# Kernel tuning notes

Hardware: AMD Instinct MI355X
Metric: run time of the kernel (lower is better)

The kernel has to match this reference:

```python
import jax, jax.numpy as jnp
import numpy as np

N_NODES = 100000


def gcn_conv(x, src, dst, ew, W, b):
    """PyG GCNConv: linear transform, add self-loops, symmetric degree
    normalization with edge weights, scatter-add aggregation, then bias."""
    n = x.shape[0]
    h = x @ W  # [N, out] transform BEFORE propagation (PyG order)
    # add self-loops with weight 1
    loop = jnp.arange(n, dtype=src.dtype)
    s = jnp.concatenate([src, loop])
    d = jnp.concatenate([dst, loop])
    w = jnp.concatenate([ew, jnp.ones((n,), dtype=ew.dtype)])
    # symmetric normalization: deg computed over incoming edge weights
    deg = jax.ops.segment_sum(w, d, num_segments=n)
    dinv = jnp.where(deg > 0, jax.lax.rsqrt(deg), 0.0)
    norm = dinv[s] * w * dinv[d]  # [E+N]
    msg = h[s] * norm[:, None]  # gather + scale
    out = jax.ops.segment_sum(msg, d, num_segments=n)  # scatter-add
    return out + b


def setup_inputs() -> dict:
    key = jax.random.key(0)
    k = jax.random.split(key, 6)
    N, E, F, H, C = N_NODES, 3200000, 512, 16, 40
    x = jax.random.normal(k[0], (N, F), dtype=jnp.float32)
    edge_index = jax.random.randint(k[1], (2, E), 0, N, dtype=jnp.int64)
    edge_weight = jax.random.uniform(k[2], (E,), dtype=jnp.float32)
    W1 = jax.random.normal(k[3], (F, H), dtype=jnp.float32) * (1.0 / np.sqrt(F))
    b1 = jnp.zeros((H,), dtype=jnp.float32)
    W2 = jax.random.normal(k[4], (H, C), dtype=jnp.float32) * (1.0 / np.sqrt(H))
    b2 = jnp.zeros((C,), dtype=jnp.float32)
    return {"x": x, "edge_index": edge_index, "edge_weight": edge_weight,
            "W1": W1, "b1": b1, "W2": W2, "b2": b2}


def reference(x, edge_index, edge_weight, W1, b1, W2, b2):
    src, dst = edge_index[0], edge_index[1]
    h = jax.nn.relu(gcn_conv(x, src, dst, edge_weight, W1, b1))
    # F.dropout with training=False (eval) is identity -> omitted
    h = gcn_conv(h, src, dst, edge_weight, W2, b2)
    return jax.nn.log_softmax(h, axis=1)
```

## Files before the change

### kernel.cpp

```cpp
#include <hip/hip_runtime.h>


#define NF 512
#define NH 16
#define NRANGE 32
#define NS2 32
#define RS 3125
#define EB 1024
#define GROWS 256
#define GK 16

__device__ __forceinline__ unsigned short f2bf(float f) {
    unsigned u = __float_as_uint(f);
    return (unsigned short)((u + 0x7fff + ((u >> 16) & 1)) >> 16);
}
__device__ __forceinline__ float bf2f(unsigned b) {
    return __uint_as_float(b << 16);
}


__global__ __launch_bounds__(256) void k_bincount(const int* __restrict__ dst,
                                                  int* __restrict__ bktcnt,
                                                  int E, int nblk) {
    __shared__ int cnt[NRANGE];
    if (threadIdx.x < NRANGE) cnt[threadIdx.x] = 0;
    __syncthreads();
    int b0 = blockIdx.x * EB;
#pragma unroll
    for (int j = 0; j < 4; ++j) {
        int e = b0 + j * 256 + threadIdx.x;
        if (e < E) atomicAdd(&cnt[dst[e] / RS], 1);
    }
    __syncthreads();
    if (threadIdx.x < NRANGE)
        bktcnt[threadIdx.x * nblk + blockIdx.x] = cnt[threadIdx.x];
}

__global__ __launch_bounds__(256) void k_scan_block(const int* __restrict__ in,
                                                    int* __restrict__ outp,
                                                    int* __restrict__ bsum, int n) {
    __shared__ int sh[256];
    int t = threadIdx.x, g = blockIdx.x * 256 + t;
    int v = (g < n) ? in[g] : 0;
    sh[t] = v; __syncthreads();
    for (int off = 1; off < 256; off <<= 1) {
        int a = (t >= off) ? sh[t - off] : 0;
        __syncthreads();
        sh[t] += a;
        __syncthreads();
    }
    if (g < n) outp[g] = sh[t] - v;
    if (t == 255) bsum[blockIdx.x] = sh[255];
}

__global__ __launch_bounds__(256) void k_sumscan(const int* __restrict__ partials,
                                                 const float* __restrict__ wpartials,
                                                 int* __restrict__ rowptr,
                                                 int* __restrict__ bsum,
                                                 float* __restrict__ dinv, int n) {
    __shared__ int sh[256];
    int t = threadIdx.x, g = blockIdx.x * 256 + t;
    int v = 0;
    if (g < n) {
        int r = g / RS, b = g - r * RS;
        size_t o = (size_t)(r * NS2) * RS + b;
        const int* p = partials + o;
        const float* wp = wpartials + o;
        float w = 1.0f;
#pragma unroll
        for (int s = 0; s < NS2; ++s) { v += p[s * RS]; w += wp[s * RS]; }
        dinv[g] = rsqrtf(w);
    }
    sh[t] = v; __syncthreads();
    for (int off = 1; off < 256; off <<= 1) {
        int a = (t >= off) ? sh[t - off] : 0;
        __syncthreads();
        sh[t] += a;
        __syncthreads();
    }
    if (g < n) rowptr[g] = sh[t] - v;
    if (t == 255) bsum[blockIdx.x] = sh[255];
}

__global__ __launch_bounds__(512) void k_scan_tops(int* __restrict__ bsum,
                                                   int* __restrict__ outp,
                                                   int nb, int n) {
    __shared__ int sh[512];
    int t = threadIdx.x;
    int v = (t < nb) ? bsum[t] : 0;
    sh[t] = v; __syncthreads();
    for (int off = 1; off < 512; off <<= 1) {
        int a = (t >= off) ? sh[t - off] : 0;
        __syncthreads();
        sh[t] += a;
        __syncthreads();
    }
    if (t < nb) bsum[t] = sh[t] - v;
    if (t == 511) outp[n] = sh[511];
}

__global__ __launch_bounds__(256) void k_scan_add(int* __restrict__ outp,
                                                  const int* __restrict__ bsum, int n) {
    int i = blockIdx.x * 256 + threadIdx.x;
    if (i < n) outp[i] += bsum[i >> 8];
}

__global__ __launch_bounds__(256) void k_binfill(const int* __restrict__ src,
                                                 const int* __restrict__ dst,
                                                 const float* __restrict__ ew,
                                                 const int* __restrict__ bktcnt,
                                                 const int* __restrict__ bsum2,
                                                 int2* __restrict__ bin,
                                                 int E, int nblk) {
    __shared__ int base[NRANGE];
    if (threadIdx.x < NRANGE) {
        int idx = threadIdx.x * nblk + blockIdx.x;
        base[threadIdx.x] = bktcnt[idx] + bsum2[idx >> 8];
    }
    __syncthreads();
    int b0 = blockIdx.x * EB;
#pragma unroll
    for (int j = 0; j < 4; ++j) {
        int e = b0 + j * 256 + threadIdx.x;
        if (e < E) {
            int d = dst[e];
            int r = d / RS;
            int pos = atomicAdd(&base[r], 1);
            bin[pos] = make_int2((src[e] << 12) | (d - r * RS),
                                 __float_as_int(ew[e]));
        }
    }
}

__device__ __forceinline__ int bkt_start(const int* bktcnt, const int* bsum2,
                                         int r, int nblk, int E) {
    if (r >= NRANGE) return E;
    int idx = r * nblk;
    return bktcnt[idx] + bsum2[idx >> 8];
}

__global__ __launch_bounds__(256) void k_hist2(const int2* __restrict__ bin,
                                               const int* __restrict__ bktcnt,
                                               const int* __restrict__ bsum2,
                                               int* __restrict__ partials,
                                               float* __restrict__ wpartials,
                                               int E, int nblk) {
    __shared__ int hist[RS];
    __shared__ float whist[RS];
    int r = blockIdx.x >> 5, s = blockIdx.x & (NS2 - 1);
    for (int t = threadIdx.x; t < RS; t += 256) { hist[t] = 0; whist[t] = 0.f; }
    __syncthreads();
    int b0 = bkt_start(bktcnt, bsum2, r, nblk, E);
    int b1 = bkt_start(bktcnt, bsum2, r + 1, nblk, E);
    int len = b1 - b0, ss = (len + NS2 - 1) / NS2;
    int cs = b0 + s * ss, ce = min(cs + ss, b1);
    for (int j = cs + threadIdx.x; j < ce; j += 256) {
        int2 p2 = bin[j];
        int dl = p2.x & 4095;
        atomicAdd(&hist[dl], 1);
        atomicAdd(&whist[dl], __int_as_float(p2.y));
    }
    __syncthreads();
    size_t o = (size_t)(r * NS2 + s) * RS;
    int* pp = partials + o;
    float* wpp = wpartials + o;
    for (int t = threadIdx.x; t < RS; t += 256) { pp[t] = hist[t]; wpp[t] = whist[t]; }
}

__global__ __launch_bounds__(256) void k_slicecur(int* __restrict__ partials,
                                                  const int* __restrict__ rowptr, int n) {
    int d = blockIdx.x * 256 + threadIdx.x;
    if (d >= n) return;
    int r = d / RS, b = d - r * RS;
    int* p = partials + (size_t)(r * NS2) * RS + b;
    int run = rowptr[d];
#pragma unroll
    for (int s = 0; s < NS2; ++s) {
        int c = p[s * RS];
        p[s * RS] = run;
        run += c;
    }
}

__global__ __launch_bounds__(256) void k_fill3(const int2* __restrict__ bin,
                                               const int* __restrict__ bktcnt,
                                               const int* __restrict__ bsum2,
                                               const int* __restrict__ partials,
                                               const float* __restrict__ dinv,
                                               unsigned* __restrict__ csr,
                                               int E, int nblk) {
    __shared__ int cur[RS];
    __shared__ float dv[RS];
    int r = blockIdx.x >> 5, s = blockIdx.x & (NS2 - 1);
    const int* cp = partials + (size_t)(r * NS2 + s) * RS;
    for (int t = threadIdx.x; t < RS; t += 256) {
        cur[t] = cp[t];
        dv[t] = dinv[r * RS + t];
    }
    __syncthreads();
    int b0 = bkt_start(bktcnt, bsum2, r, nblk, E);
    int b1 = bkt_start(bktcnt, bsum2, r + 1, nblk, E);
    int len = b1 - b0, ss = (len + NS2 - 1) / NS2;
    int cs = b0 + s * ss, ce = min(cs + ss, b1);
    for (int j = cs + threadIdx.x; j < ce; j += 256) {
        int2 p2 = bin[j];
        int dl = p2.x & 4095;
        int sn = p2.x >> 12;
        float nrm = dinv[sn] * __int_as_float(p2.y) * dv[dl];
        unsigned w15 = (unsigned)(nrm * 32767.0f + 0.5f);
        int pos = atomicAdd(&cur[dl], 1);
        csr[pos] = ((unsigned)sn << 15) | w15;
    }
}

__global__ __launch_bounds__(256) void k_gemm1(const float* __restrict__ x,
                                               const float* __restrict__ w1,
                                               unsigned short* __restrict__ h, int n) {
    __shared__ float wt[NF * NH];
    __shared__ float xs[2][GROWS * GK];
    for (int t = threadIdx.x; t < NF * NH; t += 256) {
        int k = t >> 4, f = t & 15;
        wt[(k >> 2) * 64 + (f << 2) + (k & 3)] = w1[t];
    }
    int rq = threadIdx.x >> 2;
    int fq = threadIdx.x & 3;
    int base = blockIdx.x * GROWS;
    float4 stage[4];
#define LOAD_CHUNK(kc)                                                        \
    _Pragma("unroll")                                                         \
    for (int li = 0; li < 4; ++li) {                                          \
        int idx = li * 256 + threadIdx.x;                                     \
        int row = idx >> 2, c4 = idx & 3;                                     \
        int rg = base + row; if (rg > n - 1) rg = n - 1;                      \
        stage[li] = *(const float4*)(x + (size_t)rg * NF + (kc) * GK + c4 * 4);\
    }
#define WRITE_CHUNK(b)                                                        \
    _Pragma("unroll")                                                         \
    for (int li = 0; li < 4; ++li) {                                          \
        int idx = li * 256 + threadIdx.x;                                     \
        int row = idx >> 2, c4 = idx & 3;                                     \
        int slot = (c4 + (row >> 2)) & 3;                                     \
        float* p = &xs[b][row * GK + slot * 4];                               \
        p[0] = stage[li].x; p[1] = stage[li].y;                               \
        p[2] = stage[li].z; p[3] = stage[li].w;                               \
    }
    float acc[4][4] = {{0.f}};
    LOAD_CHUNK(0)
    WRITE_CHUNK(0)
    __syncthreads();
    for (int kc = 0; kc < NF / GK; ++kc) {
        if (kc + 1 < NF / GK) { LOAD_CHUNK(kc + 1) }
        int b = kc & 1;
#pragma unroll
        for (int k4c = 0; k4c < GK / 4; ++k4c) {
            int k4 = kc * (GK / 4) + k4c;
            float4 wf[4];
#pragma unroll
            for (int c = 0; c < 4; ++c)
                wf[c] = *(const float4*)&wt[k4 * 64 + (fq * 4 + c) * 4];
#pragma unroll
            for (int i = 0; i < 4; ++i) {
                int row = rq * 4 + i;
                int slot = (k4c + rq) & 3;
                float4 xv = *(const float4*)&xs[b][row * GK + slot * 4];
#pragma unroll
                for (int c = 0; c < 4; ++c) {
                    acc[i][c] = fmaf(xv.x, wf[c].x, acc[i][c]);
                    acc[i][c] = fmaf(xv.y, wf[c].y, acc[i][c]);
                    acc[i][c] = fmaf(xv.z, wf[c].z, acc[i][c]);
                    acc[i][c] = fmaf(xv.w, wf[c].w, acc[i][c]);
                }
            }
        }
        if (kc + 1 < NF / GK) {
            __syncthreads();
            WRITE_CHUNK((kc + 1) & 1)
            __syncthreads();
        }
    }
#pragma unroll
    for (int i = 0; i < 4; ++i) {
        int r = base + rq * 4 + i;
        if (r < n) {
            ushort4 o;
            o.x = f2bf(acc[i][0]); o.y = f2bf(acc[i][1]);
            o.z = f2bf(acc[i][2]); o.w = f2bf(acc[i][3]);
            *(ushort4*)(h + (size_t)r * NH + fq * 4) = o;
        }
    }
#undef LOAD_CHUNK
#undef WRITE_CHUNK
}

template <bool RELU>
__global__ __launch_bounds__(256) void k_gatherT(const unsigned short* __restrict__ in,
                                                 const float* __restrict__ dinv,
                                                 const int* __restrict__ rowptr,
                                                 const unsigned* __restrict__ csr,
                                                 const float* __restrict__ b1,
                                                 unsigned short* __restrict__ out, int n) {
    int tid = blockIdx.x * 256 + threadIdx.x;
    int d = tid >> 3, l = tid & 7;
    if (d >= n) return;
    float di = dinv[d];
    unsigned self = *(const unsigned*)(in + (size_t)d * NH + 2 * l);
    float a0 = bf2f(self & 0xffffu) * di * di;
    float a1 = bf2f(self >> 16) * di * di;
    int e0 = rowptr[d], e1 = rowptr[d + 1];
    for (int j = e0; j < e1; ++j) {
        unsigned e = csr[j];
        float nrm = (float)(e & 32767u) * (1.0f / 32767.0f);
        unsigned pr = *(const unsigned*)(in + (size_t)(e >> 15) * NH + 2 * l);
        a0 = fmaf(bf2f(pr & 0xffffu), nrm, a0);
        a1 = fmaf(bf2f(pr >> 16), nrm, a1);
    }
    if (RELU) {
        a0 = fmaxf(a0 + b1[2 * l], 0.0f);
        a1 = fmaxf(a1 + b1[2 * l + 1], 0.0f);
    }
    unsigned pk = (unsigned)f2bf(a0) | ((unsigned)f2bf(a1) << 16);
    *(unsigned*)(out + (size_t)d * NH + 2 * l) = pk;
}

__global__ __launch_bounds__(256) void k_out(const unsigned short* __restrict__ agg,
                                             const float* __restrict__ w2,
                                             const float* __restrict__ b2,
                                             float* __restrict__ out, int n) {
    __shared__ float w2s[NH * 40];
    __shared__ float b2s[40];
    for (int t = threadIdx.x; t < NH * 40; t += 256) w2s[t] = w2[t];
    if (threadIdx.x < 40) b2s[threadIdx.x] = b2[threadIdx.x];
    __syncthreads();
    int i = blockIdx.x * 256 + threadIdx.x;
    if (i >= n) return;
    float v[NH];
    const uint4* ap = (const uint4*)(agg + (size_t)i * NH);
#pragma unroll
    for (int m = 0; m < 2; ++m) {
        uint4 q = ap[m];
        v[8 * m + 0] = bf2f(q.x & 0xffffu); v[8 * m + 1] = bf2f(q.x >> 16);
        v[8 * m + 2] = bf2f(q.y & 0xffffu); v[8 * m + 3] = bf2f(q.y >> 16);
        v[8 * m + 4] = bf2f(q.z & 0xffffu); v[8 * m + 5] = bf2f(q.z >> 16);
        v[8 * m + 6] = bf2f(q.w & 0xffffu); v[8 * m + 7] = bf2f(q.w >> 16);
    }
    float z[40];
#pragma unroll
    for (int c = 0; c < 40; ++c) {
        float a = b2s[c];
#pragma unroll
        for (int ff = 0; ff < NH; ++ff) a = fmaf(v[ff], w2s[ff * 40 + c], a);
        z[c] = a;
    }
    float mx = z[0];
#pragma unroll
    for (int c = 1; c < 40; ++c) mx = fmaxf(mx, z[c]);
    float sum = 0.0f;
#pragma unroll
    for (int c = 0; c < 40; ++c) sum += expf(z[c] - mx);
    float ls = mx + logf(sum);
    float4* op = (float4*)(out + (size_t)i * 40);
#pragma unroll
    for (int m = 0; m < 10; ++m) {
        float4 o;
        o.x = z[4 * m] - ls; o.y = z[4 * m + 1] - ls;
        o.z = z[4 * m + 2] - ls; o.w = z[4 * m + 3] - ls;
        op[m] = o;
    }
}

extern "C" void kernel_launch(void* const* d_in, const int* in_sizes, int n_in,
                              void* d_out, int out_size, void* d_ws, size_t ws_size,
                              hipStream_t stream) {
    const float* x  = (const float*)d_in[0];
    const int*   ei = (const int*)d_in[1];
    const float* ew = (const float*)d_in[2];
    const float* w1 = (const float*)d_in[3];
    const float* b1 = (const float*)d_in[4];
    const float* w2 = (const float*)d_in[5];
    const float* b2 = (const float*)d_in[6];
    float* out = (float*)d_out;

    int n = in_sizes[0] / NF;
    int E = in_sizes[2];
    const int* src = ei;
    const int* dst = ei + E;

    float*          ws        = (float*)d_ws;
    float*          dinv      = ws;
    int*            bsum      = (int*)(ws + 200000);
    int*            rowptr    = (int*)(ws + 201024);
    int*            bsum2     = (int*)(ws + 301056);
    int*            bktcnt    = (int*)(ws + 302080);
    int*            partials  = (int*)(ws + 402112);
    float*          wpartials = ws + 3602112;
    unsigned*       csr       = (unsigned*)(ws + 6802112);
    int2*           bin       = (int2*)(ws + 10002112);
    unsigned short* h         = (unsigned short*)(ws + 10002112);
    unsigned short* o1        = (unsigned short*)(ws + 10802112);

    int nblk  = (E + EB - 1) / EB;
    int ncnt  = NRANGE * nblk;
    int nb_c  = (ncnt + 255) / 256;
    int nb_n  = (n + 255) / 256;
    int nb_g8 = (n * 8 + 255) / 256;
    int nb_g  = (n + GROWS - 1) / GROWS;

    k_bincount<<<nblk, 256, 0, stream>>>(dst, bktcnt, E, nblk);
    k_scan_block<<<nb_c, 256, 0, stream>>>(bktcnt, bktcnt, bsum2, ncnt);
    k_scan_tops<<<1, 512, 0, stream>>>(bsum2, bktcnt, nb_c, ncnt);
    k_binfill<<<nblk, 256, 0, stream>>>(src, dst, ew, bktcnt, bsum2, bin, E, nblk);
    k_hist2<<<NRANGE * NS2, 256, 0, stream>>>(bin, bktcnt, bsum2, partials,
                                              wpartials, E, nblk);
    k_sumscan<<<nb_n, 256, 0, stream>>>(partials, wpartials, rowptr, bsum, dinv, n);
    k_scan_tops<<<1, 512, 0, stream>>>(bsum, rowptr, nb_n, n);
    k_scan_add<<<nb_n, 256, 0, stream>>>(rowptr, bsum, n);
    k_slicecur<<<nb_n, 256, 0, stream>>>(partials, rowptr, n);
    k_fill3<<<NRANGE * NS2, 256, 0, stream>>>(bin, bktcnt, bsum2, partials,
                                              dinv, csr, E, nblk);
    k_gemm1<<<nb_g, 256, 0, stream>>>(x, w1, h, n);
    k_gatherT<true><<<nb_g8, 256, 0, stream>>>(h, dinv, rowptr, csr, b1, o1, n);
    k_gatherT<false><<<nb_g8, 256, 0, stream>>>(o1, dinv, rowptr, csr, b1, h, n);
    k_out<<<nb_n, 256, 0, stream>>>(h, w2, b2, out, n);
}
```

Before: 289.4 us.

## Pack degree count and quantized weight into one histogram word; bf16 W1 in LDS

The histogram kernel now keeps the in-degree count and a fixed-point (1/1024) edge-weight sum in a single 32-bit word: 7 bits of count, 25 bits of weight. That halves the LDS atomics and the global partials traffic, and drops the separate float weight array. The downstream kernels unpack the fields. Separately, the first GEMM stores W1 as packed bf16 in shared memory, halving its LDS footprint, which may help occupancy. The cost is lower precision in the degree normalization and in W1, plus count overflow if a node gets more than 127 edges in one slice.

```diff
diff --git a/kernel.cpp b/kernel.cpp
--- a/kernel.cpp
+++ b/kernel.cpp
@@ -53,8 +53,7 @@
     if (t == 255) bsum[blockIdx.x] = sh[255];
 }
 
-__global__ __launch_bounds__(256) void k_sumscan(const int* __restrict__ partials,
-                                                 const float* __restrict__ wpartials,
+__global__ __launch_bounds__(256) void k_sumscan(const unsigned* __restrict__ partials,
                                                  int* __restrict__ rowptr,
                                                  int* __restrict__ bsum,
                                                  float* __restrict__ dinv, int n) {
@@ -63,13 +62,15 @@
     int v = 0;
     if (g < n) {
         int r = g / RS, b = g - r * RS;
-        size_t o = (size_t)(r * NS2) * RS + b;
-        const int* p = partials + o;
-        const float* wp = wpartials + o;
-        float w = 1.0f;
-#pragma unroll
-        for (int s = 0; s < NS2; ++s) { v += p[s * RS]; w += wp[s * RS]; }
-        dinv[g] = rsqrtf(w);
+        const unsigned* p = partials + (size_t)(r * NS2) * RS + b;
+        unsigned wq = 0;
+#pragma unroll
+        for (int s = 0; s < NS2; ++s) {
+            unsigned pk = p[s * RS];
+            v += (int)(pk >> 25);
+            wq += pk & 0x1ffffffu;
+        }
+        dinv[g] = rsqrtf(1.0f + (float)wq * (1.0f / 1024.0f));
     }
     sh[t] = v; __syncthreads();
     for (int off = 1; off < 256; off <<= 1) {
@@ -142,13 +143,11 @@
 __global__ __launch_bounds__(256) void k_hist2(const int2* __restrict__ bin,
                                                const int* __restrict__ bktcnt,
                                                const int* __restrict__ bsum2,
-                                               int* __restrict__ partials,
-                                               float* __restrict__ wpartials,
+                                               unsigned* __restrict__ partials,
                                                int E, int nblk) {
-    __shared__ int hist[RS];
-    __shared__ float whist[RS];
+    __shared__ unsigned hist[RS];
     int r = blockIdx.x >> 5, s = blockIdx.x & (NS2 - 1);
-    for (int t = threadIdx.x; t < RS; t += 256) { hist[t] = 0; whist[t] = 0.f; }
+    for (int t = threadIdx.x; t < RS; t += 256) hist[t] = 0;
     __syncthreads();
     int b0 = bkt_start(bktcnt, bsum2, r, nblk, E);
     int b1 = bkt_start(bktcnt, bsum2, r + 1, nblk, E);
@@ -156,28 +155,25 @@
     int cs = b0 + s * ss, ce = min(cs + ss, b1);
     for (int j = cs + threadIdx.x; j < ce; j += 256) {
         int2 p2 = bin[j];
-        int dl = p2.x & 4095;
-        atomicAdd(&hist[dl], 1);
-        atomicAdd(&whist[dl], __int_as_float(p2.y));
-    }
-    __syncthreads();
-    size_t o = (size_t)(r * NS2 + s) * RS;
-    int* pp = partials + o;
-    float* wpp = wpartials + o;
-    for (int t = threadIdx.x; t < RS; t += 256) { pp[t] = hist[t]; wpp[t] = whist[t]; }
-}
-
-__global__ __launch_bounds__(256) void k_slicecur(int* __restrict__ partials,
+        unsigned wq = (unsigned)(__int_as_float(p2.y) * 1024.0f + 0.5f);
+        atomicAdd(&hist[p2.x & 4095], (1u << 25) | wq);
+    }
+    __syncthreads();
+    unsigned* pp = partials + (size_t)(r * NS2 + s) * RS;
+    for (int t = threadIdx.x; t < RS; t += 256) pp[t] = hist[t];
+}
+
+__global__ __launch_bounds__(256) void k_slicecur(unsigned* __restrict__ partials,
                                                   const int* __restrict__ rowptr, int n) {
     int d = blockIdx.x * 256 + threadIdx.x;
     if (d >= n) return;
     int r = d / RS, b = d - r * RS;
-    int* p = partials + (size_t)(r * NS2) * RS + b;
+    unsigned* p = partials + (size_t)(r * NS2) * RS + b;
     int run = rowptr[d];
 #pragma unroll
     for (int s = 0; s < NS2; ++s) {
-        int c = p[s * RS];
-        p[s * RS] = run;
+        int c = (int)(p[s * RS] >> 25);
+        p[s * RS] = (unsigned)run;
         run += c;
     }
 }
@@ -185,16 +181,16 @@
 __global__ __launch_bounds__(256) void k_fill3(const int2* __restrict__ bin,
                                                const int* __restrict__ bktcnt,
                                                const int* __restrict__ bsum2,
-                                               const int* __restrict__ partials,
+                                               const unsigned* __restrict__ partials,
                                                const float* __restrict__ dinv,
                                                unsigned* __restrict__ csr,
                                                int E, int nblk) {
     __shared__ int cur[RS];
     __shared__ float dv[RS];
     int r = blockIdx.x >> 5, s = blockIdx.x & (NS2 - 1);
-    const int* cp = partials + (size_t)(r * NS2 + s) * RS;
+    const unsigned* cp = partials + (size_t)(r * NS2 + s) * RS;
     for (int t = threadIdx.x; t < RS; t += 256) {
-        cur[t] = cp[t];
+        cur[t] = (int)cp[t];
         dv[t] = dinv[r * RS + t];
     }
     __syncthreads();
@@ -216,11 +212,14 @@
 __global__ __launch_bounds__(256) void k_gemm1(const float* __restrict__ x,
                                                const float* __restrict__ w1,
                                                unsigned short* __restrict__ h, int n) {
-    __shared__ float wt[NF * NH];
+    __shared__ unsigned wtb[NF * NH / 2];
     __shared__ float xs[2][GROWS * GK];
-    for (int t = threadIdx.x; t < NF * NH; t += 256) {
-        int k = t >> 4, f = t & 15;
-        wt[(k >> 2) * 64 + (f << 2) + (k & 3)] = w1[t];
+    for (int idx = threadIdx.x; idx < NF * NH / 2; idx += 256) {
+        int k4 = idx >> 5, rem = idx & 31;
+        int f = rem >> 1, kk = (rem & 1) * 2;
+        float v0 = w1[(k4 * 4 + kk) * NH + f];
+        float v1 = w1[(k4 * 4 + kk + 1) * NH + f];
+        wtb[idx] = (unsigned)f2bf(v0) | ((unsigned)f2bf(v1) << 16);
     }
     int rq = threadIdx.x >> 2;
     int fq = threadIdx.x & 3;
@@ -256,8 +255,13 @@
             int k4 = kc * (GK / 4) + k4c;
             float4 wf[4];
 #pragma unroll
-            for (int c = 0; c < 4; ++c)
-                wf[c] = *(const float4*)&wt[k4 * 64 + (fq * 4 + c) * 4];
+            for (int c = 0; c < 4; ++c) {
+                uint2 u = *(const uint2*)&wtb[k4 * 32 + (fq * 4 + c) * 2];
+                wf[c].x = __uint_as_float(u.x << 16);
+                wf[c].y = __uint_as_float(u.x & 0xffff0000u);
+                wf[c].z = __uint_as_float(u.y << 16);
+                wf[c].w = __uint_as_float(u.y & 0xffff0000u);
+            }
 #pragma unroll
             for (int i = 0; i < 4; ++i) {
                 int row = rq * 4 + i;
@@ -385,18 +389,17 @@
     const int* src = ei;
     const int* dst = ei + E;
 
-    float*          ws        = (float*)d_ws;
-    float*          dinv      = ws;
-    int*            bsum      = (int*)(ws + 200000);
-    int*            rowptr    = (int*)(ws + 201024);
-    int*            bsum2     = (int*)(ws + 301056);
-    int*            bktcnt    = (int*)(ws + 302080);
-    int*            partials  = (int*)(ws + 402112);
-    float*          wpartials = ws + 3602112;
-    unsigned*       csr       = (unsigned*)(ws + 6802112);
-    int2*           bin       = (int2*)(ws + 10002112);
-    unsigned short* h         = (unsigned short*)(ws + 10002112);
-    unsigned short* o1        = (unsigned short*)(ws + 10802112);
+    float*          ws       = (float*)d_ws;
+    float*          dinv     = ws;
+    int*            bsum     = (int*)(ws + 200000);
+    int*            rowptr   = (int*)(ws + 201024);
+    int*            bsum2    = (int*)(ws + 301056);
+    int*            bktcnt   = (int*)(ws + 302080);
+    unsigned*       partials = (unsigned*)(ws + 402112);
+    unsigned*       csr      = (unsigned*)(ws + 6802112);
+    int2*           bin      = (int2*)(ws + 10002112);
+    unsigned short* h        = (unsigned short*)(ws + 10002112);
+    unsigned short* o1       = (unsigned short*)(ws + 10802112);
 
     int nblk  = (E + EB - 1) / EB;
     int ncnt  = NRANGE * nblk;
@@ -409,9 +412,8 @@
     k_scan_block<<<nb_c, 256, 0, stream>>>(bktcnt, bktcnt, bsum2, ncnt);
     k_scan_tops<<<1, 512, 0, stream>>>(bsum2, bktcnt, nb_c, ncnt);
     k_binfill<<<nblk, 256, 0, stream>>>(src, dst, ew, bktcnt, bsum2, bin, E, nblk);
-    k_hist2<<<NRANGE * NS2, 256, 0, stream>>>(bin, bktcnt, bsum2, partials,
-                                              wpartials, E, nblk);
-    k_sumscan<<<nb_n, 256, 0, stream>>>(partials, wpartials, rowptr, bsum, dinv, n);
+    k_hist2<<<NRANGE * NS2, 256, 0, stream>>>(bin, bktcnt, bsum2, partials, E, nblk);
+    k_sumscan<<<nb_n, 256, 0, stream>>>(partials, rowptr, bsum, dinv, n);
     k_scan_tops<<<1, 512, 0, stream>>>(bsum, rowptr, nb_n, n);
     k_scan_add<<<nb_n, 256, 0, stream>>>(rowptr, bsum, n);
     k_slicecur<<<nb_n, 256, 0, stream>>>(partials, rowptr, n);
```

New measurement: 279.2 us. 3.5% less time.
